# Kernel optimization log

Hardware: AMD Instinct MI355X
Metric: run time of the kernel (lower is better)

## Reference

```python
import jax, jax.numpy as jnp
import numpy as np

SCALE = 16.0
TEMP = 0.07
EPS = 1e-8


def setup_inputs() -> dict:
    key = jax.random.key(0)
    k0, k1, k2, k3, k4 = jax.random.split(key, 5)
    B, D, h, w = 16, 128, 48, 48
    feats_a = jax.random.normal(k0, (B, D, h, w), jnp.float32)
    feats_b = jax.random.normal(k1, (B, D, h, w), jnp.float32)
    eye = jnp.eye(3, dtype=jnp.float32)
    # near-identity homographies (must be invertible)
    Hs_a = eye[None] + 0.02 * jax.random.normal(k2, (B, 3, 3), jnp.float32)
    Hs_b = eye[None] + 0.02 * jax.random.normal(k3, (B, 3, 3), jnp.float32)
    # near-identity affine with a small translation (in large-image pixels)
    M_a_b = jnp.array([[1.0, 0.0, 24.0], [0.0, 1.0, -16.0]], jnp.float32) \
        + 0.01 * jax.random.normal(k4, (2, 3), jnp.float32)
    return {"feats_a": feats_a, "feats_b": feats_b, "Hs_a": Hs_a, "Hs_b": Hs_b, "M_a_b": M_a_b}


def _transform_matrix(Hs_a, Hs_b, M_a_b):
    # Feat_A -> Img_A -> Large_A -> Large_B -> Img_B -> Feat_B
    B = Hs_a.shape[0]
    dt = Hs_a.dtype
    M3 = jnp.concatenate([M_a_b, jnp.array([[0.0, 0.0, 1.0]], dt)], axis=0)  # (3,3)
    S = jnp.diag(jnp.array([SCALE, SCALE, 1.0], dt))
    S_inv = jnp.diag(jnp.array([1.0 / SCALE, 1.0 / SCALE, 1.0], dt))
    Ha_inv = jnp.linalg.inv(Hs_a)  # (B,3,3)
    T = S_inv[None] @ Hs_b @ M3[None] @ Ha_inv @ S[None]
    return T


def _bilinear_sample(feats, grid):
    # feats (B,D,H,W); grid (B,h,w,2) normalized to [-1,1], align_corners=True,
    # zero padding for out-of-range samples (matches F.grid_sample).
    B, D, H, W = feats.shape
    h, w = grid.shape[1], grid.shape[2]
    ix = (grid[..., 0] + 1.0) * 0.5 * (W - 1)  # (B,h,w)
    iy = (grid[..., 1] + 1.0) * 0.5 * (H - 1)
    x0 = jnp.floor(ix); y0 = jnp.floor(iy)
    wx1 = ix - x0; wx0 = 1.0 - wx1
    wy1 = iy - y0; wy0 = 1.0 - wy1
    feats_flat = feats.reshape(B, D, H * W)

    def gather(xi, yi):
        valid = (xi >= 0) & (xi <= W - 1) & (yi >= 0) & (yi <= H - 1)
        xc = jnp.clip(xi, 0, W - 1).astype(jnp.int32)
        yc = jnp.clip(yi, 0, H - 1).astype(jnp.int32)
        idx = (yc * W + xc).reshape(B, -1)  # (B, h*w)
        v = jnp.take_along_axis(feats_flat, idx[:, None, :], axis=2)  # (B,D,h*w)
        return v * valid.reshape(B, 1, -1).astype(feats.dtype)

    out = (gather(x0, y0) * (wx0 * wy0).reshape(B, 1, -1)
           + gather(x0 + 1, y0) * (wx1 * wy0).reshape(B, 1, -1)
           + gather(x0, y0 + 1) * (wx0 * wy1).reshape(B, 1, -1)
           + gather(x0 + 1, y0 + 1) * (wx1 * wy1).reshape(B, 1, -1))
    return out.reshape(B, D, h, w)


def reference(feats_a, feats_b, Hs_a, Hs_b, M_a_b):
    B, D, h, w = feats_a.shape
    N = h * w
    H_b, W_b = feats_b.shape[2], feats_b.shape[3]
    T = _transform_matrix(Hs_a, Hs_b, M_a_b)  # (B,3,3)

    # homogeneous pixel grid of feats_a: (3, N)
    gy, gx = jnp.meshgrid(jnp.arange(h, dtype=jnp.float32), jnp.arange(w, dtype=jnp.float32), indexing='ij')
    coords = jnp.stack([gx.ravel(), gy.ravel(), jnp.ones(N, jnp.float32)], axis=0)  # (3,N)
    new = jnp.einsum('bij,jn->bin', T, coords)  # (B,3,N)
    z = new[:, 2, :] + EPS
    x_norm = 2.0 * (new[:, 0, :] / z) / (W_b - 1) - 1.0  # (B,N)
    y_norm = 2.0 * (new[:, 1, :] / z) / (H_b - 1) - 1.0
    grid = jnp.stack([x_norm, y_norm], axis=-1).reshape(B, h, w, 2)
    valid_mask = ((grid[..., 0] >= -1) & (grid[..., 0] <= 1)
                  & (grid[..., 1] >= -1) & (grid[..., 1] <= 1)).astype(jnp.float32)  # (B,h,w)

    warped_b = _bilinear_sample(feats_b, grid)  # (B,D,h,w)

    fa = feats_a.reshape(B, D, N).transpose(0, 2, 1)   # (B,N,D)
    wb = warped_b.reshape(B, D, N).transpose(0, 2, 1)  # (B,N,D)
    # F.normalize: x / max(||x||, eps) with eps=1e-12
    fa = fa / jnp.maximum(jnp.linalg.norm(fa, axis=2, keepdims=True), 1e-12)
    wb = wb / jnp.maximum(jnp.linalg.norm(wb, axis=2, keepdims=True), 1e-12)

    logits = jnp.einsum('bnd,bmd->bnm', fa, wb) / TEMP  # (B,N,N)
    # cross-entropy with labels = diagonal
    lse = jax.nn.logsumexp(logits, axis=-1)  # (B,N)
    diag = jnp.einsum('bnn->bn', logits)     # (B,N)
    loss_per = lse - diag                    # (B,N)

    mask = valid_mask.reshape(B, N)
    num_valid = mask.sum()
    total = (loss_per * mask).sum()
    return jnp.where(num_valid > 0, total / jnp.maximum(num_valid, 1.0), 0.0)
```

## Files before the change

### kernel.cpp

```cpp
#include <hip/hip_runtime.h>
#include <math.h>

#define B_ 16
#define D_ 128
#define HH 48
#define WW 48
#define N_ 2304
#define NC 72
#define SCALE_ 16.0f
#define INV_TEMP 14.285714285714286f
#define L2E_TEMP 20.60992915555662f
#define EPS_ 1e-8f
#define SPLITC 6
#define STAGES 6

typedef __attribute__((ext_vector_type(8))) short bf16x8;
typedef __attribute__((ext_vector_type(16))) float f32x16;

__device__ __forceinline__ short f2bf(float f) {
    union { float f; unsigned u; } v; v.f = f;
    unsigned r = v.u + 0x7FFFu + ((v.u >> 16) & 1u);
    return (short)(r >> 16);
}

__device__ __forceinline__ size_t frag_off(int b, int c, int ks, int lane) {
    return ((((size_t)b * NC + c) * 8 + ks) << 9) + (size_t)lane * 8;
}

__global__ __launch_bounds__(256) void k_prep(const float* __restrict__ fa,
                                              const float* __restrict__ fb,
                                              const float* __restrict__ Ha,
                                              const float* __restrict__ Hb,
                                              const float* __restrict__ Mab,
                                              float* __restrict__ maskA,
                                              short* __restrict__ faF,
                                              short* __restrict__ wbF) {
    __shared__ float part[4][2][32];
    const int b = blockIdx.y;
    const int rb = blockIdx.x;
    const int n0 = rb * 32;
    const int tid = threadIdx.x;
    const int lane = tid & 63, wv = tid >> 6;
    const int r = lane & 31, h = lane >> 5;
    const int n = n0 + r;

    float T[9];
    {
        const float* A = Ha + b * 9;
        const float* Bm = Hb + b * 9;
        float c00 = A[4] * A[8] - A[5] * A[7];
        float c01 = A[5] * A[6] - A[3] * A[8];
        float c02 = A[3] * A[7] - A[4] * A[6];
        float id = 1.f / (A[0] * c00 + A[1] * c01 + A[2] * c02);
        float inv[9] = { c00 * id, (A[2] * A[7] - A[1] * A[8]) * id, (A[1] * A[5] - A[2] * A[4]) * id,
                         c01 * id, (A[0] * A[8] - A[2] * A[6]) * id, (A[2] * A[3] - A[0] * A[5]) * id,
                         c02 * id, (A[1] * A[6] - A[0] * A[7]) * id, (A[0] * A[4] - A[1] * A[3]) * id };
        float M3[9] = {Mab[0], Mab[1], Mab[2], Mab[3], Mab[4], Mab[5], 0.f, 0.f, 1.f};
        float P1[9], P2[9];
        for (int i = 0; i < 3; ++i)
            for (int j = 0; j < 3; ++j) {
                float s = 0.f;
                for (int k = 0; k < 3; ++k) s += Bm[i * 3 + k] * M3[k * 3 + j];
                P1[i * 3 + j] = s;
            }
        for (int i = 0; i < 3; ++i)
            for (int j = 0; j < 3; ++j) {
                float s = 0.f;
                for (int k = 0; k < 3; ++k) s += P1[i * 3 + k] * inv[k * 3 + j];
                P2[i * 3 + j] = s;
            }
        const float sc[3] = {SCALE_, SCALE_, 1.f};
        for (int i = 0; i < 3; ++i)
            for (int j = 0; j < 3; ++j) T[i * 3 + j] = P2[i * 3 + j] * sc[j] / sc[i];
    }

    const float gx = (float)(n % WW), gy = (float)(n / WW);
    const float X = T[0] * gx + T[1] * gy + T[2];
    const float Y = T[3] * gx + T[4] * gy + T[5];
    const float z = T[6] * gx + T[7] * gy + T[8] + EPS_;
    const float xn = 2.f * (X / z) / (float)(WW - 1) - 1.f;
    const float yn = 2.f * (Y / z) / (float)(HH - 1) - 1.f;
    const float msk = (xn >= -1.f && xn <= 1.f && yn >= -1.f && yn <= 1.f) ? 1.f : 0.f;
    const float ix = (xn + 1.f) * 0.5f * (float)(WW - 1);
    const float iy = (yn + 1.f) * 0.5f * (float)(HH - 1);
    const float x0f = floorf(ix), y0f = floorf(iy);
    const float wx1 = ix - x0f, wx0 = 1.f - wx1;
    const float wy1 = iy - y0f, wy0 = 1.f - wy1;
    const bool vx0 = (x0f >= 0.f) && (x0f <= 47.f);
    const bool vx1 = (x0f + 1.f >= 0.f) && (x0f + 1.f <= 47.f);
    const bool vy0 = (y0f >= 0.f) && (y0f <= 47.f);
    const bool vy1 = (y0f + 1.f >= 0.f) && (y0f + 1.f <= 47.f);
    const float w00 = (vx0 && vy0) ? wx0 * wy0 : 0.f;
    const float w01 = (vx1 && vy0) ? wx1 * wy0 : 0.f;
    const float w10 = (vx0 && vy1) ? wx0 * wy1 : 0.f;
    const float w11 = (vx1 && vy1) ? wx1 * wy1 : 0.f;
    const int x0c = (int)fminf(fmaxf(x0f, 0.f), 47.f);
    const int x1c = (int)fminf(fmaxf(x0f + 1.f, 0.f), 47.f);
    const int y0c = (int)fminf(fmaxf(y0f, 0.f), 47.f);
    const int y1c = (int)fminf(fmaxf(y0f + 1.f, 0.f), 47.f);
    const int o00 = y0c * WW + x0c, o01 = y0c * WW + x1c;
    const int o10 = y1c * WW + x0c, o11 = y1c * WW + x1c;

    const float* fab = fa + (size_t)b * D_ * N_;
    const float* fbb = fb + (size_t)b * D_ * N_;

    float av[2][8], wvv[2][8];
    float sA = 0.f, sW = 0.f;
    #pragma unroll
    for (int g = 0; g < 2; ++g) {
        const int ks = wv + 4 * g;
        const int dbase = ks * 16 + h * 8;
        #pragma unroll
        for (int j = 0; j < 8; ++j) {
            const int d = dbase + j;
            const float* p = fbb + (size_t)d * N_;
            float w = w00 * p[o00] + w01 * p[o01] + w10 * p[o10] + w11 * p[o11];
            float a = fab[(size_t)d * N_ + n];
            av[g][j] = a; wvv[g][j] = w;
            sA += a * a; sW += w * w;
        }
    }
    sA += __shfl_xor(sA, 32);
    sW += __shfl_xor(sW, 32);
    if (lane < 32) { part[wv][0][r] = sA; part[wv][1][r] = sW; }
    if (tid < 32) maskA[b * N_ + n0 + r] = msk;
    __syncthreads();
    const float rnA = 1.f / fmaxf(sqrtf(part[0][0][r] + part[1][0][r] + part[2][0][r] + part[3][0][r]), 1e-12f);
    const float rnW = 1.f / fmaxf(sqrtf(part[0][1][r] + part[1][1][r] + part[2][1][r] + part[3][1][r]), 1e-12f);

    #pragma unroll
    for (int g = 0; g < 2; ++g) {
        const int ks = wv + 4 * g;
        bf16x8 oa, ow;
        #pragma unroll
        for (int j = 0; j < 8; ++j) {
            oa[j] = f2bf(av[g][j] * rnA);
            ow[j] = f2bf(wvv[g][j] * rnW);
        }
        size_t off = frag_off(b, rb, ks, lane);
        *(bf16x8*)(faF + off) = oa;
        *(bf16x8*)(wbF + off) = ow;
    }
}

__global__ __launch_bounds__(256, 4) void k_loss(const short* __restrict__ faF,
                                                 const short* __restrict__ wbF,
                                                 float* __restrict__ Zpart,
                                                 float* __restrict__ dgbuf) {
    __shared__ short bbuf[2][8192];
    __shared__ float s_Z[128];
    const int bx = blockIdx.x;
    const int cs = blockIdx.y;
    const int b = blockIdx.z;
    const int tid = threadIdx.x;
    const int lane = tid & 63, w = tid >> 6;
    const int l31 = lane & 31, h = lane >> 5;
    const int rc = bx * 4 + w;

    bf16x8 af[8];
    #pragma unroll
    for (int ks = 0; ks < 8; ++ks)
        af[ks] = *(const bf16x8*)(faF + frag_off(b, rc, ks, lane));

    float Z[16];
    #pragma unroll
    for (int i = 0; i < 16; ++i) Z[i] = 0.f;

    const short* bsrc = wbF + frag_off(b, cs * 12, 0, 0);

    #pragma unroll
    for (int i = 0; i < 4; ++i)
        *(float4*)(&bbuf[0][tid * 8 + i * 2048]) = *(const float4*)(bsrc + tid * 8 + i * 2048);
    __syncthreads();

    for (int s = 0; s < STAGES; ++s) {
        float4 pf[4];
        const bool more = (s + 1 < STAGES);
        if (more) {
            const short* src = bsrc + (s + 1) * 8192;
            #pragma unroll
            for (int i = 0; i < 4; ++i) pf[i] = *(const float4*)(src + tid * 8 + i * 2048);
        }
        const short* bb = &bbuf[s & 1][0];
        f32x16 C0, C1;
        #pragma unroll
        for (int i = 0; i < 16; ++i) { C0[i] = 0.f; C1[i] = 0.f; }
        #pragma unroll
        for (int ks = 0; ks < 8; ++ks) {
            bf16x8 b0 = *(const bf16x8*)(bb + ks * 512 + lane * 8);
            bf16x8 b1 = *(const bf16x8*)(bb + 4096 + ks * 512 + lane * 8);
            C0 = __builtin_amdgcn_mfma_f32_32x32x16_bf16(af[ks], b0, C0, 0, 0, 0);
            C1 = __builtin_amdgcn_mfma_f32_32x32x16_bf16(af[ks], b1, C1, 0, 0, 0);
        }
        #pragma unroll
        for (int i = 0; i < 16; ++i) {
            Z[i] += exp2f(fmaf(C0[i], L2E_TEMP, -L2E_TEMP))
                  + exp2f(fmaf(C1[i], L2E_TEMP, -L2E_TEMP));
        }
        const int jc0 = cs * 12 + 2 * s, jc1 = jc0 + 1;
        if (jc0 == rc) {
            #pragma unroll
            for (int i = 0; i < 16; ++i) {
                int rr = (i & 3) + 8 * (i >> 2) + 4 * h;
                if (l31 == rr) dgbuf[b * N_ + rc * 32 + rr] = INV_TEMP * C0[i];
            }
        }
        if (jc1 == rc) {
            #pragma unroll
            for (int i = 0; i < 16; ++i) {
                int rr = (i & 3) + 8 * (i >> 2) + 4 * h;
                if (l31 == rr) dgbuf[b * N_ + rc * 32 + rr] = INV_TEMP * C1[i];
            }
        }
        if (more) {
            short* dst = &bbuf[(s + 1) & 1][0];
            #pragma unroll
            for (int i = 0; i < 4; ++i) *(float4*)(dst + tid * 8 + i * 2048) = pf[i];
        }
        __syncthreads();
    }

    #pragma unroll
    for (int i = 0; i < 16; ++i) {
        float z = Z[i];
        z += __shfl_xor(z, 1);
        z += __shfl_xor(z, 2);
        z += __shfl_xor(z, 4);
        z += __shfl_xor(z, 8);
        z += __shfl_xor(z, 16);
        if (l31 == 0) {
            int rr = (i & 3) + 8 * (i >> 2) + 4 * h;
            s_Z[w * 32 + rr] = z;
        }
    }
    __syncthreads();
    if (tid < 128)
        Zpart[((size_t)cs * B_ + b) * N_ + bx * 128 + tid] = s_Z[tid];
}

__global__ __launch_bounds__(256) void k_pass2(const float* __restrict__ maskA,
                                               const float* __restrict__ Zpart,
                                               const float* __restrict__ dgbuf,
                                               float* __restrict__ partials) {
    const int idx = blockIdx.x * 256 + threadIdx.x;
    float Zs = 0.f;
    #pragma unroll
    for (int s = 0; s < SPLITC; ++s) Zs += Zpart[(size_t)s * B_ * N_ + idx];
    const float m = maskA[idx];
    float lossv = (logf(Zs) + INV_TEMP - dgbuf[idx]) * m;
    float cm = m;
    for (int off = 1; off < 64; off <<= 1) {
        lossv += __shfl_xor(lossv, off);
        cm += __shfl_xor(cm, off);
    }
    __shared__ float s[8];
    const int wv = threadIdx.x >> 6;
    if ((threadIdx.x & 63) == 0) { s[wv * 2] = lossv; s[wv * 2 + 1] = cm; }
    __syncthreads();
    if (threadIdx.x == 0) {
        partials[blockIdx.x * 2] = s[0] + s[2] + s[4] + s[6];
        partials[blockIdx.x * 2 + 1] = s[1] + s[3] + s[5] + s[7];
    }
}

__global__ void k_final(const float* __restrict__ partials, float* __restrict__ out) {
    const int t = threadIdx.x;
    float tt = 0.f, cc = 0.f;
    for (int i = t; i < 144; i += 64) { tt += partials[i * 2]; cc += partials[i * 2 + 1]; }
    for (int off = 1; off < 64; off <<= 1) {
        tt += __shfl_xor(tt, off);
        cc += __shfl_xor(cc, off);
    }
    if (t == 0) out[0] = (cc > 0.f) ? tt / fmaxf(cc, 1.f) : 0.f;
}

extern "C" void kernel_launch(void* const* d_in, const int* in_sizes, int n_in,
                              void* d_out, int out_size, void* d_ws, size_t ws_size,
                              hipStream_t stream) {
    const float* fa = (const float*)d_in[0];
    const float* fb = (const float*)d_in[1];
    const float* Ha = (const float*)d_in[2];
    const float* Hb = (const float*)d_in[3];
    const float* M = (const float*)d_in[4];
    float* out = (float*)d_out;

    float* wsf = (float*)d_ws;
    float* Zpart = wsf;
    float* dgbuf = Zpart + (size_t)SPLITC * B_ * N_;
    float* maskA = dgbuf + B_ * N_;
    float* partials = maskA + B_ * N_;
    short* faF = (short*)(partials + 512);
    short* wbF = faF + (size_t)B_ * NC * 8 * 512;

    hipLaunchKernelGGL(k_prep, dim3(NC, B_), dim3(256), 0, stream,
                       fa, fb, Ha, Hb, M, maskA, faF, wbF);
    hipLaunchKernelGGL(k_loss, dim3(N_ / 128, SPLITC, B_), dim3(256), 0, stream,
                       faF, wbF, Zpart, dgbuf);
    hipLaunchKernelGGL(k_pass2, dim3(B_ * N_ / 256), dim3(256), 0, stream,
                       maskA, Zpart, dgbuf, partials);
    hipLaunchKernelGGL(k_final, dim3(1), dim3(64), 0, stream, partials, out);
}
```

Baseline: 138.9 us.

## Fuse loss reduction into GEMM kernel with atomics and fold temperature scale into features

Removes the separate pass2 and final-reduction kernels. Partial softmax denominators are now accumulated with atomics into a single buffer. The last column-split block of each row group computes that group's loss, and the last group writes the final mean. The log2(e)/T scale is folded into the normalized warped features, so the inner loop calls exp2 directly with no per-element FMA and no max shift. This trades two launches and a scratch round trip for global atomics and a larger unshifted exponent range, plus slightly different bf16 rounding.

```diff
diff --git a/kernel.cpp b/kernel.cpp
--- a/kernel.cpp
+++ b/kernel.cpp
@@ -10,9 +10,11 @@
 #define SCALE_ 16.0f
 #define INV_TEMP 14.285714285714286f
 #define L2E_TEMP 20.60992915555662f
+#define LN2_ 0.6931471805599453f
 #define EPS_ 1e-8f
 #define SPLITC 6
 #define STAGES 6
+#define NGROUP 288
 
 typedef __attribute__((ext_vector_type(8))) short bf16x8;
 typedef __attribute__((ext_vector_type(16))) float f32x16;
@@ -33,16 +35,24 @@
                                               const float* __restrict__ Hb,
                                               const float* __restrict__ Mab,
                                               float* __restrict__ maskA,
+                                              float* __restrict__ Zbuf,
+                                              int* __restrict__ cnts,
                                               short* __restrict__ faF,
                                               short* __restrict__ wbF) {
     __shared__ float part[4][2][32];
     const int b = blockIdx.y;
     const int rb = blockIdx.x;
+    const int linear = b * NC + rb;
     const int n0 = rb * 32;
     const int tid = threadIdx.x;
     const int lane = tid & 63, wv = tid >> 6;
     const int r = lane & 31, h = lane >> 5;
     const int n = n0 + r;
+
+    if (linear < 144) Zbuf[linear * 256 + tid] = 0.f;
+    if (linear == 144) {
+        for (int i = tid; i < NGROUP + 3; i += 256) cnts[i] = 0;
+    }
 
     float T[9];
     {
@@ -126,7 +136,7 @@
     if (tid < 32) maskA[b * N_ + n0 + r] = msk;
     __syncthreads();
     const float rnA = 1.f / fmaxf(sqrtf(part[0][0][r] + part[1][0][r] + part[2][0][r] + part[3][0][r]), 1e-12f);
-    const float rnW = 1.f / fmaxf(sqrtf(part[0][1][r] + part[1][1][r] + part[2][1][r] + part[3][1][r]), 1e-12f);
+    const float rnW = L2E_TEMP / fmaxf(sqrtf(part[0][1][r] + part[1][1][r] + part[2][1][r] + part[3][1][r]), 1e-12f);
 
     #pragma unroll
     for (int g = 0; g < 2; ++g) {
@@ -145,10 +155,15 @@
 
 __global__ __launch_bounds__(256, 4) void k_loss(const short* __restrict__ faF,
                                                  const short* __restrict__ wbF,
-                                                 float* __restrict__ Zpart,
-                                                 float* __restrict__ dgbuf) {
+                                                 const float* __restrict__ maskA,
+                                                 float* __restrict__ Zbuf,
+                                                 float* __restrict__ dgbuf,
+                                                 int* __restrict__ cnts,
+                                                 float* __restrict__ acc,
+                                                 float* __restrict__ out) {
     __shared__ short bbuf[2][8192];
     __shared__ float s_Z[128];
+    __shared__ int s_flag;
     const int bx = blockIdx.x;
     const int cs = blockIdx.y;
     const int b = blockIdx.z;
@@ -193,23 +208,22 @@
             C1 = __builtin_amdgcn_mfma_f32_32x32x16_bf16(af[ks], b1, C1, 0, 0, 0);
         }
         #pragma unroll
-        for (int i = 0; i < 16; ++i) {
-            Z[i] += exp2f(fmaf(C0[i], L2E_TEMP, -L2E_TEMP))
-                  + exp2f(fmaf(C1[i], L2E_TEMP, -L2E_TEMP));
-        }
+        for (int i = 0; i < 16; ++i)
+            Z[i] += exp2f(C0[i]) + exp2f(C1[i]);
+
         const int jc0 = cs * 12 + 2 * s, jc1 = jc0 + 1;
         if (jc0 == rc) {
             #pragma unroll
             for (int i = 0; i < 16; ++i) {
                 int rr = (i & 3) + 8 * (i >> 2) + 4 * h;
-                if (l31 == rr) dgbuf[b * N_ + rc * 32 + rr] = INV_TEMP * C0[i];
+                if (l31 == rr) atomicExch(&dgbuf[b * N_ + rc * 32 + rr], C0[i]);
             }
         }
         if (jc1 == rc) {
             #pragma unroll
             for (int i = 0; i < 16; ++i) {
                 int rr = (i & 3) + 8 * (i >> 2) + 4 * h;
-                if (l31 == rr) dgbuf[b * N_ + rc * 32 + rr] = INV_TEMP * C1[i];
+                if (l31 == rr) atomicExch(&dgbuf[b * N_ + rc * 32 + rr], C1[i]);
             }
         }
         if (more) {
@@ -235,43 +249,43 @@
     }
     __syncthreads();
     if (tid < 128)
-        Zpart[((size_t)cs * B_ + b) * N_ + bx * 128 + tid] = s_Z[tid];
-}
-
-__global__ __launch_bounds__(256) void k_pass2(const float* __restrict__ maskA,
-                                               const float* __restrict__ Zpart,
-                                               const float* __restrict__ dgbuf,
-                                               float* __restrict__ partials) {
-    const int idx = blockIdx.x * 256 + threadIdx.x;
-    float Zs = 0.f;
-    #pragma unroll
-    for (int s = 0; s < SPLITC; ++s) Zs += Zpart[(size_t)s * B_ * N_ + idx];
-    const float m = maskA[idx];
-    float lossv = (logf(Zs) + INV_TEMP - dgbuf[idx]) * m;
-    float cm = m;
-    for (int off = 1; off < 64; off <<= 1) {
-        lossv += __shfl_xor(lossv, off);
-        cm += __shfl_xor(cm, off);
-    }
-    __shared__ float s[8];
-    const int wv = threadIdx.x >> 6;
-    if ((threadIdx.x & 63) == 0) { s[wv * 2] = lossv; s[wv * 2 + 1] = cm; }
-    __syncthreads();
-    if (threadIdx.x == 0) {
-        partials[blockIdx.x * 2] = s[0] + s[2] + s[4] + s[6];
-        partials[blockIdx.x * 2 + 1] = s[1] + s[3] + s[5] + s[7];
-    }
-}
-
-__global__ void k_final(const float* __restrict__ partials, float* __restrict__ out) {
-    const int t = threadIdx.x;
-    float tt = 0.f, cc = 0.f;
-    for (int i = t; i < 144; i += 64) { tt += partials[i * 2]; cc += partials[i * 2 + 1]; }
-    for (int off = 1; off < 64; off <<= 1) {
-        tt += __shfl_xor(tt, off);
-        cc += __shfl_xor(cc, off);
-    }
-    if (t == 0) out[0] = (cc > 0.f) ? tt / fmaxf(cc, 1.f) : 0.f;
+        atomicAdd(&Zbuf[(size_t)b * N_ + bx * 128 + tid], s_Z[tid]);
+    __threadfence();
+    __syncthreads();
+    if (tid == 0)
+        s_flag = (atomicAdd(&cnts[b * 18 + bx], 1) == SPLITC - 1) ? 1 : 0;
+    __syncthreads();
+
+    if (s_flag) {
+        __threadfence();
+        float lossv = 0.f, cm = 0.f;
+        if (tid < 128) {
+            const int row = b * N_ + bx * 128 + tid;
+            float Zs = atomicAdd(&Zbuf[row], 0.f);
+            float dg = atomicAdd(&dgbuf[row], 0.f);
+            float m = maskA[row];
+            lossv = LN2_ * (log2f(Zs) - dg) * m;
+            cm = m;
+        }
+        for (int off = 1; off < 64; off <<= 1) {
+            lossv += __shfl_xor(lossv, off);
+            cm += __shfl_xor(cm, off);
+        }
+        if ((tid & 63) == 0) { s_Z[(tid >> 6) * 2] = lossv; s_Z[(tid >> 6) * 2 + 1] = cm; }
+        __syncthreads();
+        if (tid == 0) {
+            atomicAdd(&acc[0], s_Z[0] + s_Z[2]);
+            atomicAdd(&acc[1], s_Z[1] + s_Z[3]);
+            __threadfence();
+            int old = atomicAdd(&cnts[NGROUP], 1);
+            if (old == NGROUP - 1) {
+                __threadfence();
+                float tt = atomicAdd(&acc[0], 0.f);
+                float cc = atomicAdd(&acc[1], 0.f);
+                out[0] = (cc > 0.f) ? tt / fmaxf(cc, 1.f) : 0.f;
+            }
+        }
+    }
 }
 
 extern "C" void kernel_launch(void* const* d_in, const int* in_sizes, int n_in,
@@ -285,18 +299,16 @@
     float* out = (float*)d_out;
 
     float* wsf = (float*)d_ws;
-    float* Zpart = wsf;
-    float* dgbuf = Zpart + (size_t)SPLITC * B_ * N_;
+    float* Zbuf = wsf;
+    float* dgbuf = Zbuf + B_ * N_;
     float* maskA = dgbuf + B_ * N_;
-    float* partials = maskA + B_ * N_;
-    short* faF = (short*)(partials + 512);
+    int* cnts = (int*)(maskA + B_ * N_);
+    float* acc = (float*)(cnts + NGROUP + 1);
+    short* faF = (short*)(acc + 8);
     short* wbF = faF + (size_t)B_ * NC * 8 * 512;
 
     hipLaunchKernelGGL(k_prep, dim3(NC, B_), dim3(256), 0, stream,
-                       fa, fb, Ha, Hb, M, maskA, faF, wbF);
-    hipLaunchKernelGGL(k_loss, dim3(N_ / 128, SPLITC, B_), dim3(256), 0, stream,
-                       faF, wbF, Zpart, dgbuf);
-    hipLaunchKernelGGL(k_pass2, dim3(B_ * N_ / 256), dim3(256), 0, stream,
-                       maskA, Zpart, dgbuf, partials);
-    hipLaunchKernelGGL(k_final, dim3(1), dim3(64), 0, stream, partials, out);
-}
+                       fa, fb, Ha, Hb, M, maskA, Zbuf, cnts, faF, wbF);
+    hipLaunchKernelGGL(k_loss, dim3(18, SPLITC, B_), dim3(256), 0, stream,
+                       faF, wbF, maskA, Zbuf, dgbuf, cnts, acc, out);
+}
```

New measurement: 354.6 us. 155% more time.

## Widen loss tiles to two row blocks per wave, fold scale into features, fuse final reduce

Applied to the files above, without the earlier changes.

Each wave of the logits kernel now computes two 32-row blocks against every shared B tile, so each LDS B fragment feeds two MFMAs. This halves LDS reads per MFMA and doubles the row tile per block, with the column split retuned to 9 and 4 stages. The log2(e)/temperature factor is folded into the normalized B features during prep, which removes the per-element FMA before exp2 and rewrites the loss in log2 form. The separate final-reduction kernel is replaced by atomics and a last-block counter in pass2. The costs are higher register pressure (launch bounds lowered to 3) and reliance on atomic ordering for the final result.

```diff
diff --git a/kernel.cpp b/kernel.cpp
--- a/kernel.cpp
+++ b/kernel.cpp
@@ -10,9 +10,10 @@
 #define SCALE_ 16.0f
 #define INV_TEMP 14.285714285714286f
 #define L2E_TEMP 20.60992915555662f
+#define LN2_ 0.6931471805599453f
 #define EPS_ 1e-8f
-#define SPLITC 6
-#define STAGES 6
+#define SPLITC 9
+#define STAGES 4
 
 typedef __attribute__((ext_vector_type(8))) short bf16x8;
 typedef __attribute__((ext_vector_type(16))) float f32x16;
@@ -33,6 +34,7 @@
                                               const float* __restrict__ Hb,
                                               const float* __restrict__ Mab,
                                               float* __restrict__ maskA,
+                                              float* __restrict__ acc,
                                               short* __restrict__ faF,
                                               short* __restrict__ wbF) {
     __shared__ float part[4][2][32];
@@ -43,6 +45,8 @@
     const int lane = tid & 63, wv = tid >> 6;
     const int r = lane & 31, h = lane >> 5;
     const int n = n0 + r;
+
+    if (b == 0 && rb == 0 && tid < 4) ((int*)acc)[tid] = 0;
 
     float T[9];
     {
@@ -126,7 +130,7 @@
     if (tid < 32) maskA[b * N_ + n0 + r] = msk;
     __syncthreads();
     const float rnA = 1.f / fmaxf(sqrtf(part[0][0][r] + part[1][0][r] + part[2][0][r] + part[3][0][r]), 1e-12f);
-    const float rnW = 1.f / fmaxf(sqrtf(part[0][1][r] + part[1][1][r] + part[2][1][r] + part[3][1][r]), 1e-12f);
+    const float rnW = L2E_TEMP / fmaxf(sqrtf(part[0][1][r] + part[1][1][r] + part[2][1][r] + part[3][1][r]), 1e-12f);
 
     #pragma unroll
     for (int g = 0; g < 2; ++g) {
@@ -143,30 +147,32 @@
     }
 }
 
-__global__ __launch_bounds__(256, 4) void k_loss(const short* __restrict__ faF,
+__global__ __launch_bounds__(256, 3) void k_loss(const short* __restrict__ faF,
                                                  const short* __restrict__ wbF,
                                                  float* __restrict__ Zpart,
                                                  float* __restrict__ dgbuf) {
     __shared__ short bbuf[2][8192];
-    __shared__ float s_Z[128];
+    __shared__ float s_Z[256];
     const int bx = blockIdx.x;
     const int cs = blockIdx.y;
     const int b = blockIdx.z;
     const int tid = threadIdx.x;
-    const int lane = tid & 63, w = tid >> 6;
+    const int lane = tid & 63, wv = tid >> 6;
     const int l31 = lane & 31, h = lane >> 5;
-    const int rc = bx * 4 + w;
-
-    bf16x8 af[8];
-    #pragma unroll
-    for (int ks = 0; ks < 8; ++ks)
-        af[ks] = *(const bf16x8*)(faF + frag_off(b, rc, ks, lane));
-
-    float Z[16];
-    #pragma unroll
-    for (int i = 0; i < 16; ++i) Z[i] = 0.f;
-
-    const short* bsrc = wbF + frag_off(b, cs * 12, 0, 0);
+    const int rc0 = bx * 8 + 2 * wv, rc1 = rc0 + 1;
+
+    bf16x8 a0[8], a1[8];
+    #pragma unroll
+    for (int ks = 0; ks < 8; ++ks) {
+        a0[ks] = *(const bf16x8*)(faF + frag_off(b, rc0, ks, lane));
+        a1[ks] = *(const bf16x8*)(faF + frag_off(b, rc1, ks, lane));
+    }
+
+    float Z0[16], Z1[16];
+    #pragma unroll
+    for (int i = 0; i < 16; ++i) { Z0[i] = 0.f; Z1[i] = 0.f; }
+
+    const short* bsrc = wbF + frag_off(b, cs * 8, 0, 0);
 
     #pragma unroll
     for (int i = 0; i < 4; ++i)
@@ -182,34 +188,46 @@
             for (int i = 0; i < 4; ++i) pf[i] = *(const float4*)(src + tid * 8 + i * 2048);
         }
         const short* bb = &bbuf[s & 1][0];
-        f32x16 C0, C1;
-        #pragma unroll
-        for (int i = 0; i < 16; ++i) { C0[i] = 0.f; C1[i] = 0.f; }
-        #pragma unroll
-        for (int ks = 0; ks < 8; ++ks) {
-            bf16x8 b0 = *(const bf16x8*)(bb + ks * 512 + lane * 8);
-            bf16x8 b1 = *(const bf16x8*)(bb + 4096 + ks * 512 + lane * 8);
-            C0 = __builtin_amdgcn_mfma_f32_32x32x16_bf16(af[ks], b0, C0, 0, 0, 0);
-            C1 = __builtin_amdgcn_mfma_f32_32x32x16_bf16(af[ks], b1, C1, 0, 0, 0);
-        }
-        #pragma unroll
-        for (int i = 0; i < 16; ++i) {
-            Z[i] += exp2f(fmaf(C0[i], L2E_TEMP, -L2E_TEMP))
-                  + exp2f(fmaf(C1[i], L2E_TEMP, -L2E_TEMP));
-        }
-        const int jc0 = cs * 12 + 2 * s, jc1 = jc0 + 1;
-        if (jc0 == rc) {
-            #pragma unroll
-            for (int i = 0; i < 16; ++i) {
-                int rr = (i & 3) + 8 * (i >> 2) + 4 * h;
-                if (l31 == rr) dgbuf[b * N_ + rc * 32 + rr] = INV_TEMP * C0[i];
-            }
-        }
-        if (jc1 == rc) {
-            #pragma unroll
-            for (int i = 0; i < 16; ++i) {
-                int rr = (i & 3) + 8 * (i >> 2) + 4 * h;
-                if (l31 == rr) dgbuf[b * N_ + rc * 32 + rr] = INV_TEMP * C1[i];
+        const bool diag = (cs == bx) && (s == wv);
+
+        {
+            f32x16 C0, C1;
+            #pragma unroll
+            for (int i = 0; i < 16; ++i) { C0[i] = 0.f; C1[i] = 0.f; }
+            #pragma unroll
+            for (int ks = 0; ks < 8; ++ks) {
+                bf16x8 bfr = *(const bf16x8*)(bb + ks * 512 + lane * 8);
+                C0 = __builtin_amdgcn_mfma_f32_32x32x16_bf16(a0[ks], bfr, C0, 0, 0, 0);
+                C1 = __builtin_amdgcn_mfma_f32_32x32x16_bf16(a1[ks], bfr, C1, 0, 0, 0);
+            }
+            #pragma unroll
+            for (int i = 0; i < 16; ++i) { Z0[i] += exp2f(C0[i]); Z1[i] += exp2f(C1[i]); }
+            if (diag) {
+                #pragma unroll
+                for (int i = 0; i < 16; ++i) {
+                    int rr = (i & 3) + 8 * (i >> 2) + 4 * h;
+                    if (l31 == rr) dgbuf[b * N_ + rc0 * 32 + rr] = C0[i];
+                }
+            }
+        }
+        {
+            f32x16 C0, C1;
+            #pragma unroll
+            for (int i = 0; i < 16; ++i) { C0[i] = 0.f; C1[i] = 0.f; }
+            #pragma unroll
+            for (int ks = 0; ks < 8; ++ks) {
+                bf16x8 bfr = *(const bf16x8*)(bb + 4096 + ks * 512 + lane * 8);
+                C0 = __builtin_amdgcn_mfma_f32_32x32x16_bf16(a0[ks], bfr, C0, 0, 0, 0);
+                C1 = __builtin_amdgcn_mfma_f32_32x32x16_bf16(a1[ks], bfr, C1, 0, 0, 0);
+            }
+            #pragma unroll
+            for (int i = 0; i < 16; ++i) { Z0[i] += exp2f(C0[i]); Z1[i] += exp2f(C1[i]); }
+            if (diag) {
+                #pragma unroll
+                for (int i = 0; i < 16; ++i) {
+                    int rr = (i & 3) + 8 * (i >> 2) + 4 * h;
+                    if (l31 == rr) dgbuf[b * N_ + rc1 * 32 + rr] = C1[i];
+                }
             }
         }
         if (more) {
@@ -222,32 +240,33 @@
 
     #pragma unroll
     for (int i = 0; i < 16; ++i) {
-        float z = Z[i];
-        z += __shfl_xor(z, 1);
-        z += __shfl_xor(z, 2);
-        z += __shfl_xor(z, 4);
-        z += __shfl_xor(z, 8);
-        z += __shfl_xor(z, 16);
+        float z0 = Z0[i], z1 = Z1[i];
+        z0 += __shfl_xor(z0, 1);  z1 += __shfl_xor(z1, 1);
+        z0 += __shfl_xor(z0, 2);  z1 += __shfl_xor(z1, 2);
+        z0 += __shfl_xor(z0, 4);  z1 += __shfl_xor(z1, 4);
+        z0 += __shfl_xor(z0, 8);  z1 += __shfl_xor(z1, 8);
+        z0 += __shfl_xor(z0, 16); z1 += __shfl_xor(z1, 16);
         if (l31 == 0) {
             int rr = (i & 3) + 8 * (i >> 2) + 4 * h;
-            s_Z[w * 32 + rr] = z;
+            s_Z[wv * 64 + rr] = z0;
+            s_Z[wv * 64 + 32 + rr] = z1;
         }
     }
     __syncthreads();
-    if (tid < 128)
-        Zpart[((size_t)cs * B_ + b) * N_ + bx * 128 + tid] = s_Z[tid];
+    Zpart[((size_t)cs * B_ + b) * N_ + bx * 256 + tid] = s_Z[tid];
 }
 
 __global__ __launch_bounds__(256) void k_pass2(const float* __restrict__ maskA,
                                                const float* __restrict__ Zpart,
                                                const float* __restrict__ dgbuf,
-                                               float* __restrict__ partials) {
+                                               float* __restrict__ acc,
+                                               float* __restrict__ out) {
     const int idx = blockIdx.x * 256 + threadIdx.x;
     float Zs = 0.f;
     #pragma unroll
     for (int s = 0; s < SPLITC; ++s) Zs += Zpart[(size_t)s * B_ * N_ + idx];
     const float m = maskA[idx];
-    float lossv = (logf(Zs) + INV_TEMP - dgbuf[idx]) * m;
+    float lossv = LN2_ * (log2f(Zs) - dgbuf[idx]) * m;
     float cm = m;
     for (int off = 1; off < 64; off <<= 1) {
         lossv += __shfl_xor(lossv, off);
@@ -258,20 +277,16 @@
     if ((threadIdx.x & 63) == 0) { s[wv * 2] = lossv; s[wv * 2 + 1] = cm; }
     __syncthreads();
     if (threadIdx.x == 0) {
-        partials[blockIdx.x * 2] = s[0] + s[2] + s[4] + s[6];
-        partials[blockIdx.x * 2 + 1] = s[1] + s[3] + s[5] + s[7];
-    }
-}
-
-__global__ void k_final(const float* __restrict__ partials, float* __restrict__ out) {
-    const int t = threadIdx.x;
-    float tt = 0.f, cc = 0.f;
-    for (int i = t; i < 144; i += 64) { tt += partials[i * 2]; cc += partials[i * 2 + 1]; }
-    for (int off = 1; off < 64; off <<= 1) {
-        tt += __shfl_xor(tt, off);
-        cc += __shfl_xor(cc, off);
-    }
-    if (t == 0) out[0] = (cc > 0.f) ? tt / fmaxf(cc, 1.f) : 0.f;
+        atomicAdd(&acc[0], s[0] + s[2] + s[4] + s[6]);
+        atomicAdd(&acc[1], s[1] + s[3] + s[5] + s[7]);
+        asm volatile("s_waitcnt vmcnt(0)" ::: "memory");
+        int old = atomicAdd((int*)(acc + 2), 1);
+        if (old == 143) {
+            float tt = atomicAdd(&acc[0], 0.f);
+            float cc = atomicAdd(&acc[1], 0.f);
+            out[0] = (cc > 0.f) ? tt / fmaxf(cc, 1.f) : 0.f;
+        }
+    }
 }
 
 extern "C" void kernel_launch(void* const* d_in, const int* in_sizes, int n_in,
@@ -288,15 +303,14 @@
     float* Zpart = wsf;
     float* dgbuf = Zpart + (size_t)SPLITC * B_ * N_;
     float* maskA = dgbuf + B_ * N_;
-    float* partials = maskA + B_ * N_;
-    short* faF = (short*)(partials + 512);
+    float* acc = maskA + B_ * N_;
+    short* faF = (short*)(acc + 8);
     short* wbF = faF + (size_t)B_ * NC * 8 * 512;
 
     hipLaunchKernelGGL(k_prep, dim3(NC, B_), dim3(256), 0, stream,
-                       fa, fb, Ha, Hb, M, maskA, faF, wbF);
-    hipLaunchKernelGGL(k_loss, dim3(N_ / 128, SPLITC, B_), dim3(256), 0, stream,
+                       fa, fb, Ha, Hb, M, maskA, acc, faF, wbF);
+    hipLaunchKernelGGL(k_loss, dim3(N_ / 256, SPLITC, B_), dim3(256), 0, stream,
                        faF, wbF, Zpart, dgbuf);
     hipLaunchKernelGGL(k_pass2, dim3(B_ * N_ / 256), dim3(256), 0, stream,
-                       maskA, Zpart, dgbuf, partials);
-    hipLaunchKernelGGL(k_final, dim3(1), dim3(64), 0, stream, partials, out);
-}
+                       maskA, Zpart, dgbuf, acc, out);
+}
```

Measured after the change: 357.7 us. +157.6%, slower.

## Fold temperature scale into normalized B features and fuse final reduction via atomics

Applied to the files above, without the earlier changes.

The log2(e)/temperature factor moves into the normalization of the warped B features, so the loss kernel's inner exp loop needs only exp2 with no FMA and no max offset. The diagonal logits and the final log step are adjusted to stay in base 2. The separate final-reduction kernel is removed: pass2 blocks atomically accumulate sums and a counter, and the last block writes the output, saving one launch. Dropping the -1/T offset depends on the bounded cosine range to avoid overflow, and pre-scaling before bf16 rounding changes precision slightly.

```diff
diff --git a/kernel.cpp b/kernel.cpp
--- a/kernel.cpp
+++ b/kernel.cpp
@@ -10,6 +10,7 @@
 #define SCALE_ 16.0f
 #define INV_TEMP 14.285714285714286f
 #define L2E_TEMP 20.60992915555662f
+#define LN2_ 0.6931471805599453f
 #define EPS_ 1e-8f
 #define SPLITC 6
 #define STAGES 6
@@ -33,6 +34,7 @@
                                               const float* __restrict__ Hb,
                                               const float* __restrict__ Mab,
                                               float* __restrict__ maskA,
+                                              float* __restrict__ acc,
                                               short* __restrict__ faF,
                                               short* __restrict__ wbF) {
     __shared__ float part[4][2][32];
@@ -43,6 +45,8 @@
     const int lane = tid & 63, wv = tid >> 6;
     const int r = lane & 31, h = lane >> 5;
     const int n = n0 + r;
+
+    if (b == 0 && rb == 0 && tid < 4) ((int*)acc)[tid] = 0;
 
     float T[9];
     {
@@ -126,7 +130,7 @@
     if (tid < 32) maskA[b * N_ + n0 + r] = msk;
     __syncthreads();
     const float rnA = 1.f / fmaxf(sqrtf(part[0][0][r] + part[1][0][r] + part[2][0][r] + part[3][0][r]), 1e-12f);
-    const float rnW = 1.f / fmaxf(sqrtf(part[0][1][r] + part[1][1][r] + part[2][1][r] + part[3][1][r]), 1e-12f);
+    const float rnW = L2E_TEMP / fmaxf(sqrtf(part[0][1][r] + part[1][1][r] + part[2][1][r] + part[3][1][r]), 1e-12f);
 
     #pragma unroll
     for (int g = 0; g < 2; ++g) {
@@ -193,23 +197,22 @@
             C1 = __builtin_amdgcn_mfma_f32_32x32x16_bf16(af[ks], b1, C1, 0, 0, 0);
         }
         #pragma unroll
-        for (int i = 0; i < 16; ++i) {
-            Z[i] += exp2f(fmaf(C0[i], L2E_TEMP, -L2E_TEMP))
-                  + exp2f(fmaf(C1[i], L2E_TEMP, -L2E_TEMP));
-        }
+        for (int i = 0; i < 16; ++i)
+            Z[i] += exp2f(C0[i]) + exp2f(C1[i]);
+
         const int jc0 = cs * 12 + 2 * s, jc1 = jc0 + 1;
         if (jc0 == rc) {
             #pragma unroll
             for (int i = 0; i < 16; ++i) {
                 int rr = (i & 3) + 8 * (i >> 2) + 4 * h;
-                if (l31 == rr) dgbuf[b * N_ + rc * 32 + rr] = INV_TEMP * C0[i];
+                if (l31 == rr) dgbuf[b * N_ + rc * 32 + rr] = C0[i];
             }
         }
         if (jc1 == rc) {
             #pragma unroll
             for (int i = 0; i < 16; ++i) {
                 int rr = (i & 3) + 8 * (i >> 2) + 4 * h;
-                if (l31 == rr) dgbuf[b * N_ + rc * 32 + rr] = INV_TEMP * C1[i];
+                if (l31 == rr) dgbuf[b * N_ + rc * 32 + rr] = C1[i];
             }
         }
         if (more) {
@@ -241,13 +244,14 @@
 __global__ __launch_bounds__(256) void k_pass2(const float* __restrict__ maskA,
                                                const float* __restrict__ Zpart,
                                                const float* __restrict__ dgbuf,
-                                               float* __restrict__ partials) {
+                                               float* __restrict__ acc,
+                                               float* __restrict__ out) {
     const int idx = blockIdx.x * 256 + threadIdx.x;
     float Zs = 0.f;
     #pragma unroll
     for (int s = 0; s < SPLITC; ++s) Zs += Zpart[(size_t)s * B_ * N_ + idx];
     const float m = maskA[idx];
-    float lossv = (logf(Zs) + INV_TEMP - dgbuf[idx]) * m;
+    float lossv = LN2_ * (log2f(Zs) - dgbuf[idx]) * m;
     float cm = m;
     for (int off = 1; off < 64; off <<= 1) {
         lossv += __shfl_xor(lossv, off);
@@ -258,20 +262,16 @@
     if ((threadIdx.x & 63) == 0) { s[wv * 2] = lossv; s[wv * 2 + 1] = cm; }
     __syncthreads();
     if (threadIdx.x == 0) {
-        partials[blockIdx.x * 2] = s[0] + s[2] + s[4] + s[6];
-        partials[blockIdx.x * 2 + 1] = s[1] + s[3] + s[5] + s[7];
-    }
-}
-
-__global__ void k_final(const float* __restrict__ partials, float* __restrict__ out) {
-    const int t = threadIdx.x;
-    float tt = 0.f, cc = 0.f;
-    for (int i = t; i < 144; i += 64) { tt += partials[i * 2]; cc += partials[i * 2 + 1]; }
-    for (int off = 1; off < 64; off <<= 1) {
-        tt += __shfl_xor(tt, off);
-        cc += __shfl_xor(cc, off);
-    }
-    if (t == 0) out[0] = (cc > 0.f) ? tt / fmaxf(cc, 1.f) : 0.f;
+        atomicAdd(&acc[0], s[0] + s[2] + s[4] + s[6]);
+        atomicAdd(&acc[1], s[1] + s[3] + s[5] + s[7]);
+        asm volatile("s_waitcnt vmcnt(0)" ::: "memory");
+        int old = atomicAdd((int*)(acc + 2), 1);
+        if (old == 143) {
+            float tt = atomicAdd(&acc[0], 0.f);
+            float cc = atomicAdd(&acc[1], 0.f);
+            out[0] = (cc > 0.f) ? tt / fmaxf(cc, 1.f) : 0.f;
+        }
+    }
 }
 
 extern "C" void kernel_launch(void* const* d_in, const int* in_sizes, int n_in,
@@ -288,15 +288,14 @@
     float* Zpart = wsf;
     float* dgbuf = Zpart + (size_t)SPLITC * B_ * N_;
     float* maskA = dgbuf + B_ * N_;
-    float* partials = maskA + B_ * N_;
-    short* faF = (short*)(partials + 512);
+    float* acc = maskA + B_ * N_;
+    short* faF = (short*)(acc + 8);
     short* wbF = faF + (size_t)B_ * NC * 8 * 512;
 
     hipLaunchKernelGGL(k_prep, dim3(NC, B_), dim3(256), 0, stream,
-                       fa, fb, Ha, Hb, M, maskA, faF, wbF);
-    hipLaunchKernelGGL(k_loss, dim3(N_ / 128, SPLITC, B_), dim3(256), 0, stream,
+                       fa, fb, Ha, Hb, M, maskA, acc, faF, wbF);
+    hipLaunchKernelGGL(k_loss, dim3(18, SPLITC, B_), dim3(256), 0, stream,
                        faF, wbF, Zpart, dgbuf);
     hipLaunchKernelGGL(k_pass2, dim3(B_ * N_ / 256), dim3(256), 0, stream,
-                       maskA, Zpart, dgbuf, partials);
-    hipLaunchKernelGGL(k_final, dim3(1), dim3(64), 0, stream, partials, out);
-}
+                       maskA, Zpart, dgbuf, acc, out);
+}
```

New measurement: 141.2 us. Within noise of the previous version (+1.7%).
